# Performance work log

Hardware: AMD Instinct MI355X
Metric: run time of the kernel (lower is better)

The kernel has to match this reference:

```python
import jax, jax.numpy as jnp
import numpy as np

B, N, S, DIM, H = 128, 8, 16, 64, 4
DH = DIM // H

def setup_inputs() -> dict:
    key = jax.random.key(0)
    ks = jax.random.split(key, 10)
    return {
        "self_embeddings": jax.random.normal(ks[0], (B, N, DIM), jnp.float32),
        "ngh_user_embeddings": jax.random.normal(ks[1], (B, S, DIM), jnp.float32),
        "ngh_entity_embeddings": jax.random.normal(ks[2], (B, N, S, DIM), jnp.float32),
        "user_embeddings": jax.random.normal(ks[3], (B, DIM), jnp.float32),
        "item_embeddings": jax.random.normal(ks[4], (B, DIM), jnp.float32),
        "W_r": jax.random.normal(ks[5], (B, N, S, DIM, DIM), jnp.float32) * 0.1,
        "W_ui": jax.random.normal(ks[6], (DIM, DIM), jnp.float32) * 0.1,
        "lin_W": jax.random.normal(ks[7], (DIM, DIM), jnp.float32) * 0.1,
        "lin_b": jnp.zeros((DIM,), jnp.float32),
        "linUI_W": jax.random.normal(ks[8], (DIM, DIM), jnp.float32) * 0.1,
        "linUI_b": jnp.zeros((DIM,), jnp.float32),
        "is_item_layer": 1,
    }

def reference(self_embeddings, ngh_user_embeddings, ngh_entity_embeddings,
              user_embeddings, item_embeddings, W_r, W_ui,
              lin_W, lin_b, linUI_W, linUI_b, is_item_layer):
    scale = 1.0 / np.sqrt(float(DH))
    # ---- user-side ego embedding (agg_type='sum') ----
    # Wi[b,i] = sum_j W_ui[i,j] * item[b,j]
    Wi = item_embeddings @ W_ui.T                          # [B, DIM]
    Wi_h = Wi.reshape(B, H, DH)                            # split heads (chunks of DH)
    nghu_h = ngh_user_embeddings.reshape(B, S, H, DH)
    att_u = jnp.einsum('bhd,bshd->bhs', Wi_h, nghu_h) * scale
    att_u = jax.nn.softmax(att_u, axis=-1)                 # softmax over S
    user_ego = jnp.einsum('bhs,bshd->bhd', att_u, nghu_h).reshape(B, DIM)
    # sum-agg + linear_UI + act (dropout is identity at inference)
    item_UI = jax.nn.relu((item_embeddings + user_ego) @ linUI_W.T + linUI_b)  # [B, DIM]
    # ---- entity-side ego embedding (repr_type='sum') ----
    signal = user_embeddings + item_UI                     # [B, DIM]
    v = signal[:, None, :] * self_embeddings               # [B, N, DIM]
    # q[b,n,s,i] = sum_j W_r[b,n,s,i,j] * v[b,n,j]
    q = jnp.einsum('bnsij,bnj->bnsi', W_r, v)              # [B, N, S, DIM]
    q_h = q.reshape(B, N, S, H, DH)
    nghe_h = ngh_entity_embeddings.reshape(B, N, S, H, DH)
    att_e = jnp.einsum('bnshd,bnshd->bnhs', q_h, nghe_h) * scale
    att_e = jax.nn.softmax(att_e, axis=-1)                 # softmax over S
    entity_ego = jnp.einsum('bnhs,bnshd->bnhd', att_e, nghe_h).reshape(B, N, DIM)
    # ---- final aggregation (is_item_layer=True, agg_type='sum') ----
    agg = self_embeddings + user_ego[:, None, :] + entity_ego
    out = jax.nn.relu(agg @ lin_W.T + lin_b)               # [B, N, DIM]
    return out
```

## Files before the change

kernel.cpp:

```cpp
#include <hip/hip_runtime.h>
#include <hip/hip_bf16.h>

#define B_   128
#define N_   8
#define S_   16
#define DIM_ 64
#define H_   4
#define DH_  16

__device__ __forceinline__ float dot_row64f(const float* __restrict__ row,
                                            const float* __restrict__ v) {
    const float4* rp = (const float4*)row;
    float acc = 0.f;
#pragma unroll
    for (int m = 0; m < 16; ++m) {
        float4 u = rp[m];
        acc = fmaf(u.x, v[4 * m + 0], acc);
        acc = fmaf(u.y, v[4 * m + 1], acc);
        acc = fmaf(u.z, v[4 * m + 2], acc);
        acc = fmaf(u.w, v[4 * m + 3], acc);
    }
    return acc;
}

__device__ __forceinline__ void load_lds16(const float* g, float* lds) {
    __builtin_amdgcn_global_load_lds(
        (const __attribute__((address_space(1))) void*)g,
        (__attribute__((address_space(3))) void*)lds,
        16, 0, 0);
}

__global__ __launch_bounds__(256) void EntityAggregator_63342177681721_kernel(
    const float* __restrict__ self_e,
    const float* __restrict__ nghu,
    const float* __restrict__ nghe,
    const float* __restrict__ user_e,
    const float* __restrict__ item_e,
    const float* __restrict__ W_r,
    const float* __restrict__ W_ui,
    const float* __restrict__ lin_W,
    const float* __restrict__ lin_b,
    const float* __restrict__ linUI_W,
    const float* __restrict__ linUI_b,
    float* __restrict__ out)
{
    const int blk  = blockIdx.x;
    const int b    = blk >> 3;
    const int t    = threadIdx.x;
    const int w    = t >> 6;
    const int lane = t & 63;

    __shared__ __align__(16) float sW[4 * 2 * 2048];
    __shared__ float sU[S_][DIM_ + 1];
    __shared__ float sE[S_][DIM_ + 1];
    __shared__ float sQ[S_][DIM_ + 1];
    __shared__ float sItem[DIM_];
    __shared__ float sWi[DIM_];
    __shared__ float sAtt[H_][S_];
    __shared__ float sUei[DIM_];
    __shared__ float sTi[DIM_];
    __shared__ __align__(16) float sV[DIM_];
    __shared__ float sAgg[DIM_];

    const float* Wp = W_r + (size_t)blk * (S_ * DIM_ * DIM_);

    {
        const float* g = Wp + w * 16384 + lane * 4;
        float* l = sW + (w << 1) * 2048;
#pragma unroll
        for (int rr = 0; rr < 8; ++rr)
            load_lds16(g + rr * 256, l + rr * 256);
    }

    {
        const int e0 = t * 4;
        const int s  = e0 >> 6;
        const int c  = e0 & 63;
        float4 uu = *(const float4*)(nghu + (size_t)b * S_ * DIM_ + e0);
        sU[s][c + 0] = uu.x; sU[s][c + 1] = uu.y;
        sU[s][c + 2] = uu.z; sU[s][c + 3] = uu.w;
        float4 ee = *(const float4*)(nghe + (size_t)blk * S_ * DIM_ + e0);
        sE[s][c + 0] = ee.x; sE[s][c + 1] = ee.y;
        sE[s][c + 2] = ee.z; sE[s][c + 3] = ee.w;
        if (t < DIM_) sItem[t] = item_e[(size_t)b * DIM_ + t];
    }
    __syncthreads();

    if (t < DIM_) sWi[t] = dot_row64f(W_ui + t * DIM_, sItem);
    __syncthreads();

    if (t < DIM_) {
        const int h = t >> 4, s = t & 15;
        float l = 0.f;
#pragma unroll
        for (int d = 0; d < DH_; ++d) l = fmaf(sWi[h * DH_ + d], sU[s][h * DH_ + d], l);
        l *= 0.25f;
        float mx = l;
#pragma unroll
        for (int off = 8; off; off >>= 1) mx = fmaxf(mx, __shfl_xor(mx, off, 16));
        float e = __expf(l - mx);
        float sm = e;
#pragma unroll
        for (int off = 8; off; off >>= 1) sm += __shfl_xor(sm, off, 16);
        sAtt[h][s] = e / sm;
    }
    __syncthreads();

    if (t < DIM_) {
        const int h = t >> 4;
        float ego = 0.f;
#pragma unroll
        for (int s = 0; s < S_; ++s) ego = fmaf(sAtt[h][s], sU[s][t], ego);
        sUei[t] = ego;
        sTi[t]  = sItem[t] + ego;
    }
    __syncthreads();

    if (t < DIM_) {
        float a   = dot_row64f(linUI_W + t * DIM_, sTi) + linUI_b[t];
        float iui = fmaxf(a, 0.f);
        float sig = user_e[(size_t)b * DIM_ + t] + iui;
        sV[t] = sig * self_e[(size_t)blk * DIM_ + t];
    }
    __syncthreads();

    {
        const int r    = lane >> 1;
        const int half = lane & 1;
        const float4* vv4 = (const float4*)sV;
#pragma unroll 1
        for (int c = 0; c < 8; ++c) {
            if (c < 7) {
                const float* g = Wp + w * 16384 + (c + 1) * 2048 + lane * 4;
                float* lb = sW + (((w << 1) | ((c + 1) & 1))) * 2048;
#pragma unroll
                for (int rr = 0; rr < 8; ++rr)
                    load_lds16(g + rr * 256, lb + rr * 256);
                asm volatile("s_waitcnt vmcnt(8)" ::: "memory");
            } else {
                asm volatile("s_waitcnt vmcnt(0)" ::: "memory");
            }
            const float4* bp = (const float4*)(sW + (((w << 1) | (c & 1))) * 2048);
            float acc = 0.f;
#pragma unroll
            for (int m = 0; m < 8; ++m) {
                const int col4 = half * 8 + ((m + r) & 7);
                float4 u = bp[r * 16 + col4];
                float4 v = vv4[col4];
                acc = fmaf(u.x, v.x, acc);
                acc = fmaf(u.y, v.y, acc);
                acc = fmaf(u.z, v.z, acc);
                acc = fmaf(u.w, v.w, acc);
            }
            acc += __shfl_xor(acc, 1);
            if (half == 0) {
                const int rowg = w * 256 + c * 32 + r;
                sQ[rowg >> 6][rowg & 63] = acc;
            }
        }
    }
    __syncthreads();

    if (t < DIM_) {
        const int h = t >> 4, s = t & 15;
        float l = 0.f;
#pragma unroll
        for (int d = 0; d < DH_; ++d) l = fmaf(sQ[s][h * DH_ + d], sE[s][h * DH_ + d], l);
        l *= 0.25f;
        float mx = l;
#pragma unroll
        for (int off = 8; off; off >>= 1) mx = fmaxf(mx, __shfl_xor(mx, off, 16));
        float e = __expf(l - mx);
        float sm = e;
#pragma unroll
        for (int off = 8; off; off >>= 1) sm += __shfl_xor(sm, off, 16);
        sAtt[h][s] = e / sm;
    }
    __syncthreads();

    if (t < DIM_) {
        const int h = t >> 4;
        float ego = 0.f;
#pragma unroll
        for (int s = 0; s < S_; ++s) ego = fmaf(sAtt[h][s], sE[s][t], ego);
        sAgg[t] = self_e[(size_t)blk * DIM_ + t] + sUei[t] + ego;
    }
    __syncthreads();

    if (t < DIM_) {
        float o = dot_row64f(lin_W + t * DIM_, sAgg) + lin_b[t];
        o = fmaxf(o, 0.f);
        out[(size_t)blk * DIM_ + t] = o;
    }
}

extern "C" void kernel_launch(void* const* d_in, const int* in_sizes, int n_in,
                              void* d_out, int out_size, void* d_ws, size_t ws_size,
                              hipStream_t stream) {
    (void)in_sizes; (void)n_in; (void)d_ws; (void)ws_size; (void)out_size;
    const float* self_e  = (const float*)d_in[0];
    const float* nghu    = (const float*)d_in[1];
    const float* nghe    = (const float*)d_in[2];
    const float* user_e  = (const float*)d_in[3];
    const float* item_e  = (const float*)d_in[4];
    const float* W_r     = (const float*)d_in[5];
    const float* W_ui    = (const float*)d_in[6];
    const float* lin_W   = (const float*)d_in[7];
    const float* lin_b   = (const float*)d_in[8];
    const float* linUI_W = (const float*)d_in[9];
    const float* linUI_b = (const float*)d_in[10];

    dim3 grid(B_ * N_);
    dim3 block(256);
    hipLaunchKernelGGL(EntityAggregator_63342177681721_kernel, grid, block, 0, stream,
                       self_e, nghu, nghe, user_e, item_e, W_r, W_ui,
                       lin_W, lin_b, linUI_W, linUI_b, (float*)d_out);
}
```

Measured before the change: 383.7 us.

## Stream W_r through registers with double buffering instead of LDS async loads

Replaces the global_load_lds staging of W_r chunks into shared memory with direct float4 loads into two register buffers, ping-ponged across the eight row chunks. The v vector is also hoisted into registers once. This drops the 64KB LDS buffer, so more blocks can be resident (launch bounds now request 4 blocks per SIMD group). In exchange, each thread reads 128 contiguous bytes per row, which coalesces less well than the old lane-strided pattern, and register pressure rises.

```diff
diff --git a/kernel.cpp b/kernel.cpp
--- a/kernel.cpp
+++ b/kernel.cpp
@@ -23,14 +23,34 @@
     return acc;
 }
 
-__device__ __forceinline__ void load_lds16(const float* g, float* lds) {
-    __builtin_amdgcn_global_load_lds(
-        (const __attribute__((address_space(1))) void*)g,
-        (__attribute__((address_space(3))) void*)lds,
-        16, 0, 0);
-}
-
-__global__ __launch_bounds__(256) void EntityAggregator_63342177681721_kernel(
+__device__ __forceinline__ float fma4(float4 u, float4 v, float a) {
+    a = fmaf(u.x, v.x, a);
+    a = fmaf(u.y, v.y, a);
+    a = fmaf(u.z, v.z, a);
+    a = fmaf(u.w, v.w, a);
+    return a;
+}
+
+#define LOAD8(BUF, IT) do {                                                  \
+    const float4* gp_ = (const float4*)(gbase + (IT) * 2048);                \
+    BUF##0 = gp_[0]; BUF##1 = gp_[1]; BUF##2 = gp_[2]; BUF##3 = gp_[3];      \
+    BUF##4 = gp_[4]; BUF##5 = gp_[5]; BUF##6 = gp_[6]; BUF##7 = gp_[7];      \
+} while (0)
+
+#define STEP8(BUF, IT) do {                                                  \
+    float acc_ = 0.f;                                                        \
+    acc_ = fma4(BUF##0, vr0, acc_); acc_ = fma4(BUF##1, vr1, acc_);          \
+    acc_ = fma4(BUF##2, vr2, acc_); acc_ = fma4(BUF##3, vr3, acc_);          \
+    acc_ = fma4(BUF##4, vr4, acc_); acc_ = fma4(BUF##5, vr5, acc_);          \
+    acc_ = fma4(BUF##6, vr6, acc_); acc_ = fma4(BUF##7, vr7, acc_);          \
+    acc_ += __shfl_xor(acc_, 1);                                             \
+    if (half == 0) {                                                         \
+        const int rowg_ = w * 256 + (IT) * 32 + r;           \
+        sQ[rowg_ >> 6][rowg_ & 63] = acc_;                                   \
+    }                                                                        \
+} while (0)
+
+__global__ __launch_bounds__(256, 4) void EntityAggregator_63342177681721_kernel(
     const float* __restrict__ self_e,
     const float* __restrict__ nghu,
     const float* __restrict__ nghe,
@@ -50,7 +70,6 @@
     const int w    = t >> 6;
     const int lane = t & 63;
 
-    __shared__ __align__(16) float sW[4 * 2 * 2048];
     __shared__ float sU[S_][DIM_ + 1];
     __shared__ float sE[S_][DIM_ + 1];
     __shared__ float sQ[S_][DIM_ + 1];
@@ -63,14 +82,14 @@
     __shared__ float sAgg[DIM_];
 
     const float* Wp = W_r + (size_t)blk * (S_ * DIM_ * DIM_);
-
-    {
-        const float* g = Wp + w * 16384 + lane * 4;
-        float* l = sW + (w << 1) * 2048;
-#pragma unroll
-        for (int rr = 0; rr < 8; ++rr)
-            load_lds16(g + rr * 256, l + rr * 256);
-    }
+    const int r    = lane >> 1;
+    const int half = lane & 1;
+    const float* gbase = Wp + (size_t)(w * 256 + r) * 64 + half * 32;
+
+    float4 a0, a1, a2, a3, a4, a5, a6, a7;
+    float4 b0, b1, b2, b3, b4, b5, b6, b7;
+
+    LOAD8(a, 0);
 
     {
         const int e0 = t * 4;
@@ -125,39 +144,21 @@
     __syncthreads();
 
     {
-        const int r    = lane >> 1;
-        const int half = lane & 1;
         const float4* vv4 = (const float4*)sV;
-#pragma unroll 1
-        for (int c = 0; c < 8; ++c) {
-            if (c < 7) {
-                const float* g = Wp + w * 16384 + (c + 1) * 2048 + lane * 4;
-                float* lb = sW + (((w << 1) | ((c + 1) & 1))) * 2048;
-#pragma unroll
-                for (int rr = 0; rr < 8; ++rr)
-                    load_lds16(g + rr * 256, lb + rr * 256);
-                asm volatile("s_waitcnt vmcnt(8)" ::: "memory");
-            } else {
-                asm volatile("s_waitcnt vmcnt(0)" ::: "memory");
-            }
-            const float4* bp = (const float4*)(sW + (((w << 1) | (c & 1))) * 2048);
-            float acc = 0.f;
-#pragma unroll
-            for (int m = 0; m < 8; ++m) {
-                const int col4 = half * 8 + ((m + r) & 7);
-                float4 u = bp[r * 16 + col4];
-                float4 v = vv4[col4];
-                acc = fmaf(u.x, v.x, acc);
-                acc = fmaf(u.y, v.y, acc);
-                acc = fmaf(u.z, v.z, acc);
-                acc = fmaf(u.w, v.w, acc);
-            }
-            acc += __shfl_xor(acc, 1);
-            if (half == 0) {
-                const int rowg = w * 256 + c * 32 + r;
-                sQ[rowg >> 6][rowg & 63] = acc;
-            }
-        }
+        float4 vr0 = vv4[half * 8 + 0], vr1 = vv4[half * 8 + 1];
+        float4 vr2 = vv4[half * 8 + 2], vr3 = vv4[half * 8 + 3];
+        float4 vr4 = vv4[half * 8 + 4], vr5 = vv4[half * 8 + 5];
+        float4 vr6 = vv4[half * 8 + 6], vr7 = vv4[half * 8 + 7];
+
+        LOAD8(b, 1);
+        STEP8(a, 0); LOAD8(a, 2);
+        STEP8(b, 1); LOAD8(b, 3);
+        STEP8(a, 2); LOAD8(a, 4);
+        STEP8(b, 3); LOAD8(b, 5);
+        STEP8(a, 4); LOAD8(a, 6);
+        STEP8(b, 5); LOAD8(b, 7);
+        STEP8(a, 6);
+        STEP8(b, 7);
     }
     __syncthreads();
 
```

Result: no change. 383.9 us (+0.1%).
